# Kernel tuning notes

Measured on AMD Instinct MI355X. Metric: run time of the kernel, lower is better.

The kernel has to match this reference:

```python
import jax, jax.numpy as jnp
import numpy as np

H_HEADS = 16
STATE_N = 64

def setup_inputs() -> dict:
    key = jax.random.key(0)
    ks = jax.random.split(key, 9)
    B, T, D = 2, 1024, 1024
    H, ch, N = H_HEADS, D // H_HEADS, STATE_N
    inp = jax.random.normal(ks[0], (B, T, D), dtype=jnp.float32)
    # lin_logA params scaled so exp(cumsum(logA)) stays bounded (decaying state)
    W_logA = jax.random.normal(ks[1], (H, 1, ch), dtype=jnp.float32) * 0.01
    b_logA = jnp.full((H, 1), -0.05, dtype=jnp.float32)
    W_XBC = jax.random.normal(ks[3], (H, ch + 2 * N, ch), dtype=jnp.float32) * (1.0 / np.sqrt(ch))
    b_XBC = jax.random.normal(ks[4], (H, ch + 2 * N), dtype=jnp.float32) * 0.02
    W_gate = jax.random.normal(ks[5], (H, ch, ch), dtype=jnp.float32) * (1.0 / np.sqrt(ch))
    b_gate = jax.random.normal(ks[6], (H, ch), dtype=jnp.float32) * 0.02
    W_out = jax.random.normal(ks[7], (D, D), dtype=jnp.float32) * (1.0 / np.sqrt(D))
    b_out = jax.random.normal(ks[8], (D,), dtype=jnp.float32) * 0.02
    return {"inp": inp, "W_logA": W_logA, "b_logA": b_logA, "W_XBC": W_XBC,
            "b_XBC": b_XBC, "W_gate": W_gate, "b_gate": b_gate,
            "W_out": W_out, "b_out": b_out}

def _mamba2_forward(inp, W_logA, b_logA, W_XBC, b_XBC, W_gate, b_gate, W_out, b_out):
    B, T, D = inp.shape
    H, N = H_HEADS, STATE_N
    ch = D // H
    x = inp.reshape(B, T, H, ch)  # B,T,H,ch
    # MultiheadLinear: matmul((H,out,in), x[...,None]) + bias
    logA = jnp.einsum('hoc,bthc->btho', W_logA, x)[..., 0] + b_logA[:, 0]  # B,T,H
    XBC = jax.nn.silu(jnp.einsum('hoc,bthc->btho', W_XBC, x) + b_XBC)     # B,T,H,ch+2N
    X = XBC[..., :ch]                 # B,T,H,ch
    Bm = XBC[..., ch:ch + N]          # B,T,H,N
    Cm = XBC[..., ch + N:]            # B,T,H,N
    # quadratic SSM: A_ss[b,h,i,j] = exp(cum[i]-cum[j]) for j<=i else 0
    cum = jnp.cumsum(jnp.swapaxes(logA, 1, 2), axis=-1)  # B,H,T
    diff = cum[..., :, None] - cum[..., None, :]          # B,H,T,T
    causal = jnp.tril(jnp.ones((T, T), dtype=bool))
    A_ss = jnp.where(causal, jnp.exp(jnp.where(causal, diff, 0.0)), 0.0)  # B,H,T,T
    G = jnp.einsum('bihn,bjhn->bhij', Cm, Bm)             # B,H,T,T (C_i . B_j)
    Y = jnp.einsum('bhij,bjhc->bihc', A_ss * G, X)        # B,T,H,ch
    gate = jnp.einsum('hoc,bthc->btho', W_gate, x) + b_gate
    Yg = (gate * Y).reshape(B, T, D)
    return Yg @ W_out.T + b_out

def reference(inp, W_logA, b_logA, W_XBC, b_XBC, W_gate, b_gate, W_out, b_out):
    return _mamba2_forward(inp, W_logA, b_logA, W_XBC, b_XBC, W_gate, b_gate, W_out, b_out)
```

## Files before the change

kernel.cpp:

```cpp
#include <hip/hip_runtime.h>

typedef unsigned int   u32;
typedef unsigned short u16;
typedef __attribute__((ext_vector_type(8))) short bf16x8;
typedef __attribute__((ext_vector_type(4))) float f32x4;

__device__ __forceinline__ float bfs(u16 u) {
  union { u32 i; float f; } v; v.i = ((u32)u) << 16; return v.f;
}
__device__ __forceinline__ u16 f2bf(float f) {
  union { float f; u32 i; } v; v.f = f;
  u32 r = v.i + 0x7fffu + ((v.i >> 16) & 1u);
  return (u16)(r >> 16);
}
__device__ __forceinline__ ushort4 f2bf4(float4 v) {
  ushort4 p; p.x = f2bf(v.x); p.y = f2bf(v.y); p.z = f2bf(v.z); p.w = f2bf(v.w);
  return p;
}

__global__ __launch_bounds__(256) void k_proj(
    const float* __restrict__ inp,
    const float* __restrict__ W_XBC,  const float* __restrict__ b_XBC,
    const float* __restrict__ W_gate, const float* __restrict__ b_gate,
    const float* __restrict__ W_logA, const float* __restrict__ b_logA,
    const float* __restrict__ Wout, u16* __restrict__ WoutB,
    u16* __restrict__ XsT, u16* __restrict__ BmsT, u16* __restrict__ CmsT,
    u16* __restrict__ gatesP, float* __restrict__ lexp, float* __restrict__ linv,
    float* __restrict__ decArr, float* __restrict__ G)
{
  int tt = blockIdx.x, h = blockIdx.y;
  int tid = threadIdx.x;
  int w = tid >> 6, l = tid & 63, q = l >> 4, lr = l & 15;
  int m0 = tt * 64;
  int b = m0 >> 10, tl0 = m0 & 1023;
  int bh = b * 16 + h;
  int jt = tt & 15;

  __shared__ u16 Xt[64][72];
  __shared__ u16 Wt[256][72];
  __shared__ float wl[64];
  __shared__ float sg[64];

  {
    int fid = h * 32 + tt;
    const float4* src = (const float4*)Wout + (size_t)fid * 512;
    ushort4* dst = (ushort4*)WoutB + (size_t)fid * 512;
    for (int i = tid; i < 512; i += 256) dst[i] = f2bf4(src[i]);
  }

  if (tid < 64) wl[tid] = W_logA[h * 64 + tid];
#pragma unroll
  for (int i = 0; i < 4; ++i) {
    int f = tid + 256 * i; int r = f >> 4, cq = f & 15;
    float4 xv = *(const float4*)(inp + (size_t)(m0 + r) * 1024 + h * 64 + 4 * cq);
    *(ushort4*)&Xt[r][4 * cq] = f2bf4(xv);
  }
#pragma unroll
  for (int i = 0; i < 16; ++i) {
    int f = tid + 256 * i; int r = f >> 4, cq = f & 15;
    const float* ws = (r < 192) ? (W_XBC + ((size_t)h * 192 + r) * 64)
                                : (W_gate + ((size_t)h * 64 + (r - 192)) * 64);
    *(ushort4*)&Wt[r][4 * cq] = f2bf4(*(const float4*)(ws + 4 * cq));
  }
  __syncthreads();

  bf16x8 af[4][2];
#pragma unroll
  for (int rt = 0; rt < 4; ++rt) {
    af[rt][0] = *(const bf16x8*)&Xt[16 * rt + lr][q * 8];
    af[rt][1] = *(const bf16x8*)&Xt[16 * rt + lr][32 + q * 8];
  }

  f32x4 acc[4][4];
#pragma unroll
  for (int rt = 0; rt < 4; ++rt)
#pragma unroll
    for (int ct = 0; ct < 4; ++ct) acc[rt][ct] = (f32x4){0.f, 0.f, 0.f, 0.f};

#pragma unroll
  for (int ct = 0; ct < 4; ++ct) {
    bf16x8 b0 = *(const bf16x8*)&Wt[64 * w + 16 * ct + lr][q * 8];
    bf16x8 b1 = *(const bf16x8*)&Wt[64 * w + 16 * ct + lr][32 + q * 8];
#pragma unroll
    for (int rt = 0; rt < 4; ++rt) {
      acc[rt][ct] = __builtin_amdgcn_mfma_f32_16x16x32_bf16(af[rt][0], b0, acc[rt][ct], 0, 0, 0);
      acc[rt][ct] = __builtin_amdgcn_mfma_f32_16x16x32_bf16(af[rt][1], b1, acc[rt][ct], 0, 0, 0);
    }
  }

  if (tid < 64) {
    float a = b_logA[h];
#pragma unroll 16
    for (int k = 0; k < 64; ++k) a += bfs(Xt[tid][k]) * wl[k];
    float lv = a;
#pragma unroll
    for (int off = 1; off < 64; off <<= 1) {
      float n = __shfl_up(lv, off, 64);
      if (tid >= off) lv += n;
    }
    float L = __shfl(lv, 63, 64);
    sg[tid] = __expf(L - lv);
    lexp[(size_t)bh * 1024 + tl0 + tid] = __expf(lv);
    linv[(size_t)bh * 1024 + tl0 + tid] = __expf(-lv);
    if (tid == 63) decArr[bh * 16 + jt] = __expf(L);
  }

  if (w < 3) {
#pragma unroll
    for (int ct = 0; ct < 4; ++ct) {
      float bias = b_XBC[h * 192 + 64 * w + 16 * ct + lr];
#pragma unroll
      for (int rt = 0; rt < 4; ++rt)
#pragma unroll
        for (int r = 0; r < 4; ++r) {
          float s = acc[rt][ct][r] + bias;
          acc[rt][ct][r] = s / (1.f + __expf(-s));
        }
    }
  } else {
#pragma unroll
    for (int ct = 0; ct < 4; ++ct) {
      float bias = b_gate[h * 64 + 16 * ct + lr];
#pragma unroll
      for (int rt = 0; rt < 4; ++rt)
#pragma unroll
        for (int r = 0; r < 4; ++r) acc[rt][ct][r] += bias;
    }
  }
  __syncthreads();

  {
    u16* T = &Wt[64 * w][0];
#pragma unroll
    for (int ct = 0; ct < 4; ++ct)
#pragma unroll
      for (int rt = 0; rt < 4; ++rt)
#pragma unroll
        for (int r = 0; r < 4; ++r) {
          int t = 16 * rt + 4 * q + r, n = 16 * ct + lr;
          u16 v = f2bf(acc[rt][ct][r]);
          if (w < 3) T[n * 72 + t] = v;
          else       T[t * 72 + n] = v;
        }
  }
  __syncthreads();

  {
#pragma unroll
    for (int i = 0; i < 16; ++i) {
      int s = l + 64 * i; int row = s >> 4, cq = s & 15;
      ushort4 v = *(ushort4*)&Wt[64 * w + row][4 * cq];
      if (w == 0)
        *(ushort4*)(XsT + ((size_t)bh * 64 + row) * 1024 + tl0 + 4 * cq) = v;
      else if (w == 1)
        *(ushort4*)(BmsT + ((size_t)bh * 64 + row) * 1024 + tl0 + 4 * cq) = v;
      else if (w == 2)
        *(ushort4*)(CmsT + ((size_t)bh * 64 + row) * 1024 + tl0 + 4 * cq) = v;
      else
        *(ushort4*)(gatesP + ((size_t)bh * 1024 + tl0 + row) * 64 + 4 * cq) = v;
    }
  }

  {
    bf16x8 a0r = *(const bf16x8*)&Wt[16 * w + lr][q * 8];
    bf16x8 a1r = *(const bf16x8*)&Wt[16 * w + lr][32 + q * 8];
    bf16x8 a0, a1;
#pragma unroll
    for (int jj = 0; jj < 8; ++jj) {
      a0[jj] = (short)f2bf(bfs((u16)a0r[jj]) * sg[q * 8 + jj]);
      a1[jj] = (short)f2bf(bfs((u16)a1r[jj]) * sg[32 + q * 8 + jj]);
    }
    f32x4 gacc[4];
#pragma unroll
    for (int nt = 0; nt < 4; ++nt) {
      gacc[nt] = (f32x4){0.f, 0.f, 0.f, 0.f};
      bf16x8 bb0 = *(const bf16x8*)&Wt[64 + 16 * nt + lr][q * 8];
      bf16x8 bb1 = *(const bf16x8*)&Wt[64 + 16 * nt + lr][32 + q * 8];
      gacc[nt] = __builtin_amdgcn_mfma_f32_16x16x32_bf16(a0, bb0, gacc[nt], 0, 0, 0);
      gacc[nt] = __builtin_amdgcn_mfma_f32_16x16x32_bf16(a1, bb1, gacc[nt], 0, 0, 0);
    }
    float* Gt = G + ((size_t)bh * 16 + jt) * 4096;
#pragma unroll
    for (int nt = 0; nt < 4; ++nt)
#pragma unroll
      for (int r = 0; r < 4; ++r)
        Gt[(16 * w + 4 * q + r) * 64 + 16 * nt + lr] = gacc[nt][r];
  }
}

__global__ __launch_bounds__(1024) void k_mid(
    const float* __restrict__ G, const float* __restrict__ decArr,
    u16* __restrict__ HpreT)
{
  int cc = blockIdx.x, bh = blockIdx.y;
  int tid = threadIdx.x;
  int e = cc * 1024 + tid;
  __shared__ float dsm[16];
  if (tid < 16) dsm[tid] = decArr[bh * 16 + tid];
  __syncthreads();
  const float* Gb = G + (size_t)bh * 16 * 4096 + e;
  float g[16];
#pragma unroll
  for (int jtl = 0; jtl < 16; ++jtl) g[jtl] = Gb[(size_t)jtl * 4096];
  u16* Hb = HpreT + (size_t)bh * 16 * 4096 + e;
  float hst = 0.f;
#pragma unroll
  for (int jtl = 0; jtl < 16; ++jtl) {
    Hb[(size_t)jtl * 4096] = f2bf(hst);
    hst = dsm[jtl] * hst + g[jtl];
  }
}

__global__ __launch_bounds__(256) void k_ssm2(
    const u16* __restrict__ XsT, const u16* __restrict__ BmsT,
    const u16* __restrict__ CmsT,
    const float* __restrict__ lexp, const float* __restrict__ linv,
    const u16* __restrict__ HpreT, const u16* __restrict__ gatesP,
    u16* __restrict__ Yg)
{
  int it = blockIdx.x, bh = blockIdx.y;
  int b = bh >> 4, h = bh & 15;
  int tid = threadIdx.x;
  int w = tid >> 6, l = tid & 63, q = l >> 4, lr = l & 15;
  int i0 = it * 64;

  __shared__ u16 Cts[64][72];
  __shared__ u16 Bts[64][72];
  __shared__ u16 Xts[64][72];
  __shared__ u16 HTt[64][72];
  __shared__ u16 Gts[64][72];
  __shared__ u16 Sts[64][72];
  __shared__ float ref_[64], cef[64];

  const u16* Xb  = XsT  + (size_t)bh * 64 * 1024;
  const u16* BbT = BmsT + (size_t)bh * 64 * 1024;
  const u16* CbT = CmsT + (size_t)bh * 64 * 1024;
  const u16* Hb  = HpreT + ((size_t)bh * 16 + it) * 4096;
  const u16* Gb  = gatesP + ((size_t)bh * 1024 + i0) * 64;

#pragma unroll
  for (int i = 0; i < 4; ++i) {
    int f = tid + 256 * i; int r = f >> 4, cq = f & 15;
    *(ushort4*)&Xts[r][4 * cq] = *(const ushort4*)(Xb + (size_t)r * 1024 + i0 + 4 * cq);
    *(ushort4*)&HTt[r][4 * cq] = *(const ushort4*)(Hb + r * 64 + 4 * cq);
    *(ushort4*)&Gts[r][4 * cq] = *(const ushort4*)(Gb + r * 64 + 4 * cq);
    ushort4 bv = *(const ushort4*)(BbT + (size_t)r * 1024 + i0 + 4 * cq);
    Bts[4 * cq + 0][r] = bv.x; Bts[4 * cq + 1][r] = bv.y;
    Bts[4 * cq + 2][r] = bv.z; Bts[4 * cq + 3][r] = bv.w;
    ushort4 cv = *(const ushort4*)(CbT + (size_t)r * 1024 + i0 + 4 * cq);
    Cts[4 * cq + 0][r] = cv.x; Cts[4 * cq + 1][r] = cv.y;
    Cts[4 * cq + 2][r] = cv.z; Cts[4 * cq + 3][r] = cv.w;
  }
  if (tid < 64) {
    ref_[tid] = lexp[(size_t)bh * 1024 + i0 + tid];
    cef[tid]  = linv[(size_t)bh * 1024 + i0 + tid];
  }
  __syncthreads();

  bf16x8 ca0 = *(const bf16x8*)&Cts[16 * w + lr][q * 8];
  bf16x8 ca1 = *(const bf16x8*)&Cts[16 * w + lr][32 + q * 8];

#pragma unroll
  for (int ct = 0; ct < 4; ++ct) {
    f32x4 s = (f32x4){0.f, 0.f, 0.f, 0.f};
    bf16x8 b0 = *(const bf16x8*)&Bts[16 * ct + lr][q * 8];
    bf16x8 b1 = *(const bf16x8*)&Bts[16 * ct + lr][32 + q * 8];
    s = __builtin_amdgcn_mfma_f32_16x16x32_bf16(ca0, b0, s, 0, 0, 0);
    s = __builtin_amdgcn_mfma_f32_16x16x32_bf16(ca1, b1, s, 0, 0, 0);
    int jl = 16 * ct + lr;
    float cj = cef[jl];
#pragma unroll
    for (int r = 0; r < 4; ++r) {
      int il = 16 * w + q * 4 + r;
      float v = (jl > il) ? 0.f : s[r] * ref_[il] * cj;
      Sts[il][jl] = f2bf(v);
    }
  }

  bf16x8 sa0 = *(const bf16x8*)&Sts[16 * w + lr][q * 8];
  bf16x8 sa1 = *(const bf16x8*)&Sts[16 * w + lr][32 + q * 8];
  f32x4 accd[4], acco[4];
#pragma unroll
  for (int ct = 0; ct < 4; ++ct) {
    accd[ct] = (f32x4){0.f, 0.f, 0.f, 0.f};
    acco[ct] = (f32x4){0.f, 0.f, 0.f, 0.f};
    bf16x8 x0 = *(const bf16x8*)&Xts[16 * ct + lr][q * 8];
    bf16x8 x1 = *(const bf16x8*)&Xts[16 * ct + lr][32 + q * 8];
    accd[ct] = __builtin_amdgcn_mfma_f32_16x16x32_bf16(sa0, x0, accd[ct], 0, 0, 0);
    accd[ct] = __builtin_amdgcn_mfma_f32_16x16x32_bf16(sa1, x1, accd[ct], 0, 0, 0);
    bf16x8 h0 = *(const bf16x8*)&HTt[16 * ct + lr][q * 8];
    bf16x8 h1 = *(const bf16x8*)&HTt[16 * ct + lr][32 + q * 8];
    acco[ct] = __builtin_amdgcn_mfma_f32_16x16x32_bf16(ca0, h0, acco[ct], 0, 0, 0);
    acco[ct] = __builtin_amdgcn_mfma_f32_16x16x32_bf16(ca1, h1, acco[ct], 0, 0, 0);
  }

#pragma unroll
  for (int ct = 0; ct < 4; ++ct) {
    int c = 16 * ct + lr;
#pragma unroll
    for (int r = 0; r < 4; ++r) {
      int il = 16 * w + q * 4 + r;
      int tg = i0 + il;
      size_t row = (size_t)(b * 1024 + tg);
      float y = accd[ct][r] + ref_[il] * acco[ct][r];
      float gt = bfs(Gts[il][c]);
      Yg[row * 1024 + h * 64 + c] = f2bf(y * gt);
    }
  }
}

__global__ __launch_bounds__(512) void k_out(
    const u16* __restrict__ Yg, const u16* __restrict__ WoutB,
    const float* __restrict__ bout, float* __restrict__ out)
{
  int bm = blockIdx.x, bn = blockIdx.y;
  int tid = threadIdx.x;
  int w = tid >> 6, l = tid & 63, q = l >> 4, lr = l & 15;
  int m0 = bm * 128, d0 = bn * 64;

  __shared__ u16 Yt[128][72];
  __shared__ u16 Wt[64][72];

  f32x4 acc[4];
#pragma unroll
  for (int ct = 0; ct < 4; ++ct) acc[ct] = (f32x4){0.f, 0.f, 0.f, 0.f};

  ushort4 py[4], pw[2];
#pragma unroll
  for (int i = 0; i < 4; ++i) {
    int f = tid + 512 * i; int r = f >> 4, cq = f & 15;
    py[i] = *(const ushort4*)(Yg + (size_t)(m0 + r) * 1024 + 4 * cq);
  }
#pragma unroll
  for (int i = 0; i < 2; ++i) {
    int f = tid + 512 * i; int r = f >> 4, cq = f & 15;
    pw[i] = *(const ushort4*)(WoutB + (size_t)(d0 + r) * 1024 + 4 * cq);
  }

  for (int kt = 0; kt < 16; ++kt) {
    __syncthreads();
#pragma unroll
    for (int i = 0; i < 4; ++i) {
      int f = tid + 512 * i; int r = f >> 4, cq = f & 15;
      *(ushort4*)&Yt[r][4 * cq] = py[i];
    }
#pragma unroll
    for (int i = 0; i < 2; ++i) {
      int f = tid + 512 * i; int r = f >> 4, cq = f & 15;
      *(ushort4*)&Wt[r][4 * cq] = pw[i];
    }
    __syncthreads();

    if (kt < 15) {
      int k1 = (kt + 1) * 64;
#pragma unroll
      for (int i = 0; i < 4; ++i) {
        int f = tid + 512 * i; int r = f >> 4, cq = f & 15;
        py[i] = *(const ushort4*)(Yg + (size_t)(m0 + r) * 1024 + k1 + 4 * cq);
      }
#pragma unroll
      for (int i = 0; i < 2; ++i) {
        int f = tid + 512 * i; int r = f >> 4, cq = f & 15;
        pw[i] = *(const ushort4*)(WoutB + (size_t)(d0 + r) * 1024 + k1 + 4 * cq);
      }
    }

    bf16x8 a0 = *(const bf16x8*)&Yt[16 * w + lr][q * 8];
    bf16x8 a1 = *(const bf16x8*)&Yt[16 * w + lr][32 + q * 8];
#pragma unroll
    for (int ct = 0; ct < 4; ++ct) {
      bf16x8 b0 = *(const bf16x8*)&Wt[16 * ct + lr][q * 8];
      bf16x8 b1 = *(const bf16x8*)&Wt[16 * ct + lr][32 + q * 8];
      acc[ct] = __builtin_amdgcn_mfma_f32_16x16x32_bf16(a0, b0, acc[ct], 0, 0, 0);
      acc[ct] = __builtin_amdgcn_mfma_f32_16x16x32_bf16(a1, b1, acc[ct], 0, 0, 0);
    }
  }

#pragma unroll
  for (int ct = 0; ct < 4; ++ct) {
    int d = d0 + 16 * ct + lr;
    float bo = bout[d];
#pragma unroll
    for (int r = 0; r < 4; ++r) {
      int m = m0 + 16 * w + q * 4 + r;
      out[(size_t)m * 1024 + d] = acc[ct][r] + bo;
    }
  }
}

extern "C" void kernel_launch(void* const* d_in, const int* in_sizes, int n_in,
                              void* d_out, int out_size, void* d_ws, size_t ws_size,
                              hipStream_t stream)
{
  const float* inp   = (const float*)d_in[0];
  const float* WlogA = (const float*)d_in[1];
  const float* blogA = (const float*)d_in[2];
  const float* WXBC  = (const float*)d_in[3];
  const float* bXBC  = (const float*)d_in[4];
  const float* Wgate = (const float*)d_in[5];
  const float* bgate = (const float*)d_in[6];
  const float* Wout  = (const float*)d_in[7];
  const float* bout  = (const float*)d_in[8];
  float* out = (float*)d_out;

  const size_t SZ = (size_t)2 * 16 * 1024 * 64;
  float* lexp   = (float*)d_ws;
  float* linv   = lexp + 32768;
  float* decA   = linv + 32768;
  float* G      = decA + 512;
  u16* base16 = (u16*)(G + (size_t)32 * 16 * 4096);
  u16* XsT    = base16;
  u16* BmsT   = XsT + SZ;
  u16* CmsT   = BmsT + SZ;
  u16* gatesP = CmsT + SZ;
  u16* Yg     = gatesP + SZ;
  u16* WoutB  = Yg + SZ;
  u16* HpreT  = WoutB + 1024 * 1024;

  k_proj<<<dim3(32, 16), 256, 0, stream>>>(inp, WXBC, bXBC, Wgate, bgate,
                                           WlogA, blogA, Wout, WoutB,
                                           XsT, BmsT, CmsT, gatesP,
                                           lexp, linv, decA, G);
  k_mid<<<dim3(4, 32), 1024, 0, stream>>>(G, decA, HpreT);
  k_ssm2<<<dim3(16, 32), 256, 0, stream>>>(XsT, BmsT, CmsT, lexp, linv,
                                           HpreT, gatesP, Yg);
  k_out<<<dim3(16, 16), 512, 0, stream>>>(Yg, WoutB, bout, out);
}
```

Before: 118.4 us.

## Fuse inter-chunk state recurrence into SSM kernel and shrink output GEMM tile

Removes the separate k_mid kernel: each k_ssm2 block now rebuilds its starting state by summing the decayed chunk states G of all earlier chunks directly from global memory, and writes the result into shared memory. This drops one kernel launch and the HpreT round trip through memory, at the cost of redundant quadratic work, since later chunks reread up to 15 chunk-state tiles. A missing barrier between the Sts writes and their reads is also added. Separately, k_out switches to 64x64 tiles with 256 threads and twice as many blocks, to improve occupancy and load balance.

```diff
diff --git a/kernel.cpp b/kernel.cpp
--- a/kernel.cpp
+++ b/kernel.cpp
@@ -188,35 +188,12 @@
   }
 }
 
-__global__ __launch_bounds__(1024) void k_mid(
-    const float* __restrict__ G, const float* __restrict__ decArr,
-    u16* __restrict__ HpreT)
-{
-  int cc = blockIdx.x, bh = blockIdx.y;
-  int tid = threadIdx.x;
-  int e = cc * 1024 + tid;
-  __shared__ float dsm[16];
-  if (tid < 16) dsm[tid] = decArr[bh * 16 + tid];
-  __syncthreads();
-  const float* Gb = G + (size_t)bh * 16 * 4096 + e;
-  float g[16];
-#pragma unroll
-  for (int jtl = 0; jtl < 16; ++jtl) g[jtl] = Gb[(size_t)jtl * 4096];
-  u16* Hb = HpreT + (size_t)bh * 16 * 4096 + e;
-  float hst = 0.f;
-#pragma unroll
-  for (int jtl = 0; jtl < 16; ++jtl) {
-    Hb[(size_t)jtl * 4096] = f2bf(hst);
-    hst = dsm[jtl] * hst + g[jtl];
-  }
-}
-
 __global__ __launch_bounds__(256) void k_ssm2(
     const u16* __restrict__ XsT, const u16* __restrict__ BmsT,
     const u16* __restrict__ CmsT,
     const float* __restrict__ lexp, const float* __restrict__ linv,
-    const u16* __restrict__ HpreT, const u16* __restrict__ gatesP,
-    u16* __restrict__ Yg)
+    const float* __restrict__ G, const float* __restrict__ decArr,
+    const u16* __restrict__ gatesP, u16* __restrict__ Yg)
 {
   int it = blockIdx.x, bh = blockIdx.y;
   int b = bh >> 4, h = bh & 15;
@@ -230,19 +207,23 @@
   __shared__ u16 HTt[64][72];
   __shared__ u16 Gts[64][72];
   __shared__ u16 Sts[64][72];
-  __shared__ float ref_[64], cef[64];
+  __shared__ float ref_[64], cef[64], dsm[16];
 
   const u16* Xb  = XsT  + (size_t)bh * 64 * 1024;
   const u16* BbT = BmsT + (size_t)bh * 64 * 1024;
   const u16* CbT = CmsT + (size_t)bh * 64 * 1024;
-  const u16* Hb  = HpreT + ((size_t)bh * 16 + it) * 4096;
   const u16* Gb  = gatesP + ((size_t)bh * 1024 + i0) * 64;
-
+  const float* Gf = G + (size_t)bh * 16 * 4096;
+
+  if (tid < 16) dsm[tid] = decArr[bh * 16 + tid];
+  if (tid < 64) {
+    ref_[tid] = lexp[(size_t)bh * 1024 + i0 + tid];
+    cef[tid]  = linv[(size_t)bh * 1024 + i0 + tid];
+  }
 #pragma unroll
   for (int i = 0; i < 4; ++i) {
     int f = tid + 256 * i; int r = f >> 4, cq = f & 15;
     *(ushort4*)&Xts[r][4 * cq] = *(const ushort4*)(Xb + (size_t)r * 1024 + i0 + 4 * cq);
-    *(ushort4*)&HTt[r][4 * cq] = *(const ushort4*)(Hb + r * 64 + 4 * cq);
     *(ushort4*)&Gts[r][4 * cq] = *(const ushort4*)(Gb + r * 64 + 4 * cq);
     ushort4 bv = *(const ushort4*)(BbT + (size_t)r * 1024 + i0 + 4 * cq);
     Bts[4 * cq + 0][r] = bv.x; Bts[4 * cq + 1][r] = bv.y;
@@ -251,15 +232,37 @@
     Cts[4 * cq + 0][r] = cv.x; Cts[4 * cq + 1][r] = cv.y;
     Cts[4 * cq + 2][r] = cv.z; Cts[4 * cq + 3][r] = cv.w;
   }
-  if (tid < 64) {
-    ref_[tid] = lexp[(size_t)bh * 1024 + i0 + tid];
-    cef[tid]  = linv[(size_t)bh * 1024 + i0 + tid];
-  }
   __syncthreads();
+
+  {
+    float hacc[4][4];
+#pragma unroll
+    for (int k = 0; k < 4; ++k)
+#pragma unroll
+      for (int r = 0; r < 4; ++r) hacc[k][r] = 0.f;
+    float fdec = 1.f;
+    for (int jt = it - 1; jt >= 0; --jt) {
+      const float* Gj = Gf + (size_t)jt * 4096 + tid * 4;
+#pragma unroll
+      for (int k = 0; k < 4; ++k) {
+        float4 g4 = *(const float4*)(Gj + 1024 * k);
+        hacc[k][0] += fdec * g4.x; hacc[k][1] += fdec * g4.y;
+        hacc[k][2] += fdec * g4.z; hacc[k][3] += fdec * g4.w;
+      }
+      fdec *= dsm[jt];
+    }
+    int row0 = tid >> 4, colb = (tid & 15) * 4;
+#pragma unroll
+    for (int k = 0; k < 4; ++k) {
+      ushort4 hv;
+      hv.x = f2bf(hacc[k][0]); hv.y = f2bf(hacc[k][1]);
+      hv.z = f2bf(hacc[k][2]); hv.w = f2bf(hacc[k][3]);
+      *(ushort4*)&HTt[row0 + 16 * k][colb] = hv;
+    }
+  }
 
   bf16x8 ca0 = *(const bf16x8*)&Cts[16 * w + lr][q * 8];
   bf16x8 ca1 = *(const bf16x8*)&Cts[16 * w + lr][32 + q * 8];
-
 #pragma unroll
   for (int ct = 0; ct < 4; ++ct) {
     f32x4 s = (f32x4){0.f, 0.f, 0.f, 0.f};
@@ -276,6 +279,7 @@
       Sts[il][jl] = f2bf(v);
     }
   }
+  __syncthreads();
 
   bf16x8 sa0 = *(const bf16x8*)&Sts[16 * w + lr][q * 8];
   bf16x8 sa1 = *(const bf16x8*)&Sts[16 * w + lr][32 + q * 8];
@@ -309,31 +313,27 @@
   }
 }
 
-__global__ __launch_bounds__(512) void k_out(
+__global__ __launch_bounds__(256) void k_out(
     const u16* __restrict__ Yg, const u16* __restrict__ WoutB,
     const float* __restrict__ bout, float* __restrict__ out)
 {
   int bm = blockIdx.x, bn = blockIdx.y;
   int tid = threadIdx.x;
   int w = tid >> 6, l = tid & 63, q = l >> 4, lr = l & 15;
-  int m0 = bm * 128, d0 = bn * 64;
-
-  __shared__ u16 Yt[128][72];
+  int m0 = bm * 64, d0 = bn * 64;
+
+  __shared__ u16 Yt[64][72];
   __shared__ u16 Wt[64][72];
 
   f32x4 acc[4];
 #pragma unroll
   for (int ct = 0; ct < 4; ++ct) acc[ct] = (f32x4){0.f, 0.f, 0.f, 0.f};
 
-  ushort4 py[4], pw[2];
+  ushort4 py[4], pw[4];
 #pragma unroll
   for (int i = 0; i < 4; ++i) {
-    int f = tid + 512 * i; int r = f >> 4, cq = f & 15;
+    int f = tid + 256 * i; int r = f >> 4, cq = f & 15;
     py[i] = *(const ushort4*)(Yg + (size_t)(m0 + r) * 1024 + 4 * cq);
-  }
-#pragma unroll
-  for (int i = 0; i < 2; ++i) {
-    int f = tid + 512 * i; int r = f >> 4, cq = f & 15;
     pw[i] = *(const ushort4*)(WoutB + (size_t)(d0 + r) * 1024 + 4 * cq);
   }
 
@@ -341,12 +341,8 @@
     __syncthreads();
 #pragma unroll
     for (int i = 0; i < 4; ++i) {
-      int f = tid + 512 * i; int r = f >> 4, cq = f & 15;
+      int f = tid + 256 * i; int r = f >> 4, cq = f & 15;
       *(ushort4*)&Yt[r][4 * cq] = py[i];
-    }
-#pragma unroll
-    for (int i = 0; i < 2; ++i) {
-      int f = tid + 512 * i; int r = f >> 4, cq = f & 15;
       *(ushort4*)&Wt[r][4 * cq] = pw[i];
     }
     __syncthreads();
@@ -355,12 +351,8 @@
       int k1 = (kt + 1) * 64;
 #pragma unroll
       for (int i = 0; i < 4; ++i) {
-        int f = tid + 512 * i; int r = f >> 4, cq = f & 15;
+        int f = tid + 256 * i; int r = f >> 4, cq = f & 15;
         py[i] = *(const ushort4*)(Yg + (size_t)(m0 + r) * 1024 + k1 + 4 * cq);
-      }
-#pragma unroll
-      for (int i = 0; i < 2; ++i) {
-        int f = tid + 512 * i; int r = f >> 4, cq = f & 15;
         pw[i] = *(const ushort4*)(WoutB + (size_t)(d0 + r) * 1024 + k1 + 4 * cq);
       }
     }
@@ -415,14 +407,12 @@
   u16* gatesP = CmsT + SZ;
   u16* Yg     = gatesP + SZ;
   u16* WoutB  = Yg + SZ;
-  u16* HpreT  = WoutB + 1024 * 1024;
 
   k_proj<<<dim3(32, 16), 256, 0, stream>>>(inp, WXBC, bXBC, Wgate, bgate,
                                            WlogA, blogA, Wout, WoutB,
                                            XsT, BmsT, CmsT, gatesP,
                                            lexp, linv, decA, G);
-  k_mid<<<dim3(4, 32), 1024, 0, stream>>>(G, decA, HpreT);
   k_ssm2<<<dim3(16, 32), 256, 0, stream>>>(XsT, BmsT, CmsT, lexp, linv,
-                                           HpreT, gatesP, Yg);
-  k_out<<<dim3(16, 16), 512, 0, stream>>>(Yg, WoutB, bout, out);
-}
+                                           G, decA, gatesP, Yg);
+  k_out<<<dim3(32, 16), 256, 0, stream>>>(Yg, WoutB, bout, out);
+}
```

New measurement: 120.1 us. About the same (+1.4%).
